# Kernel optimization log

Hardware: AMD Instinct MI355X
Metric: run time of the kernel (lower is better)

## Reference

```python
import jax, jax.numpy as jnp
import numpy as np

DECAY = 0.99
EPS = 1e-12  # torch F.normalize eps


def setup_inputs() -> dict:
    key = jax.random.key(0)
    ks = jax.random.split(key, 5)
    B, S, H, M = 4, 4096, 1024, 256
    x = jax.random.normal(ks[0], (B, S, H), dtype=jnp.float32)
    Wq = jax.random.normal(ks[1], (M, H), dtype=jnp.float32) * (H ** -0.5)
    Wk = jax.random.normal(ks[2], (M, H), dtype=jnp.float32) * (H ** -0.5)
    Wv = jax.random.normal(ks[3], (M, H), dtype=jnp.float32) * (H ** -0.5)
    # original inits W_out to zeros; use small random weights so the baseline output is non-trivial
    Wo = jax.random.normal(ks[4], (H, M), dtype=jnp.float32) * (M ** -0.5)
    M0 = jnp.zeros((M, M), dtype=jnp.float32)
    return {"x": x, "Wq": Wq, "Wk": Wk, "Wv": Wv, "Wo": Wo, "M0": M0, "chunk_size": 64}


def _l2norm(t):
    return t / jnp.maximum(jnp.linalg.norm(t, axis=-1, keepdims=True), EPS)


def reference(x, Wq, Wk, Wv, Wo, M0, chunk_size):
    B, S, H = x.shape
    m = Wq.shape[0]
    q = jnp.einsum('bsh,mh->bsm', x, Wq)
    k = _l2norm(jnp.einsum('bsh,mh->bsm', x, Wk))
    v = _l2norm(jnp.einsum('bsh,mh->bsm', x, Wv))
    n_chunks = S // chunk_size
    # (n_chunks, B, c, m)
    qc = q.reshape(B, n_chunks, chunk_size, m).transpose(1, 0, 2, 3)
    kc = k.reshape(B, n_chunks, chunk_size, m).transpose(1, 0, 2, 3)
    vc = v.reshape(B, n_chunks, chunk_size, m).transpose(1, 0, 2, 3)
    decay_c = DECAY ** chunk_size
    scale = 1.0 / (B * chunk_size)

    def step(M, qkv):
        qch, kch, vch = qkv
        r = jnp.einsum('bcm,nm->bcn', qch, M)  # q @ M.T
        outer = jnp.einsum('bci,bcj->ij', vch, kch) * scale
        return decay_c * M + outer, r

    _, rs = jax.lax.scan(step, M0, (qc, kc, vc))  # rs: (n_chunks, B, c, m)
    retrieved = rs.transpose(1, 0, 2, 3).reshape(B, S, m)
    return jnp.einsum('bsm,hm->bsh', retrieved, Wo)
```

## Files before the change

### kernel.cpp

```cpp
#include <hip/hip_runtime.h>
#include <math.h>

#define BB 4
#define SS 4096
#define HH 1024
#define MM 256
#define CHUNK 64
#define NCHUNK 64
#define ROWS (BB*SS)
#define QKV_LD 768
#define DECAY_F 0.99

typedef unsigned short u16;
typedef __attribute__((ext_vector_type(8))) short bf16x8;
typedef __attribute__((ext_vector_type(8))) unsigned short u16x8;
typedef __attribute__((ext_vector_type(4))) float f32x4;

__device__ inline u16 f2b(float f) {
  union { float f; unsigned u; } v; v.f = f;
  unsigned r = v.u + 0x7FFF + ((v.u >> 16) & 1);
  return (u16)(r >> 16);
}
__device__ inline float b2f(u16 h) {
  union { unsigned u; float f; } v; v.u = ((unsigned)h) << 16; return v.f;
}

__device__ inline void gload16(const void* g, void* l) {
  __builtin_amdgcn_global_load_lds(
      (const __attribute__((address_space(1))) unsigned int*)g,
      (__attribute__((address_space(3))) unsigned int*)l, 16, 0, 0);
}

__global__ __launch_bounds__(256) void cast_x_kernel(const float* __restrict__ src,
                                                     u16* __restrict__ dst) {
  int i = blockIdx.x * 256 + threadIdx.x;
  float4 v = reinterpret_cast<const float4*>(src)[i];
  ushort4 o;
  o.x = f2b(v.x); o.y = f2b(v.y); o.z = f2b(v.z); o.w = f2b(v.w);
  reinterpret_cast<ushort4*>(dst)[i] = o;
}

__global__ __launch_bounds__(256) void cast_w_kernel(const float* __restrict__ Wq,
                                                     const float* __restrict__ Wk,
                                                     const float* __restrict__ Wv,
                                                     const float* __restrict__ Wo,
                                                     u16* __restrict__ Wqkv_b,
                                                     u16* __restrict__ Wo_b) {
  int b = blockIdx.x, which = b >> 8;
  int i = ((b & 255) << 8) + threadIdx.x;
  const float* src = which == 0 ? Wq : which == 1 ? Wk : which == 2 ? Wv : Wo;
  u16* dst = which < 3 ? Wqkv_b + which * (MM * HH) : Wo_b;
  float4 v = reinterpret_cast<const float4*>(src)[i];
  ushort4 o;
  o.x = f2b(v.x); o.y = f2b(v.y); o.z = f2b(v.z); o.w = f2b(v.w);
  reinterpret_cast<ushort4*>(dst)[i] = o;
}

#define M_STD_BF16 0
#define M_STD_F32  1
#define M_OUTER    2
#define M_RETR     3

template<int MODE>
__global__ __launch_bounds__(256) void gemm128(const u16* __restrict__ A,
                                               const u16* __restrict__ Bg,
                                               const float* __restrict__ Bf,
                                               void* __restrict__ Cv,
                                               int K, int lda, int ldb, int ldc,
                                               float scale) {
  __shared__ bf16x8 As[2][512];
  __shared__ bf16x8 Bs[2][512];
  const int tid = threadIdx.x, lane = tid & 63, wv = tid >> 6;
  const int wr = wv >> 1, wc = wv & 1;
  const int t = (MODE == M_OUTER || MODE == M_RETR) ? blockIdx.z : 0;

  int bx, by;
  if (MODE == M_STD_BF16 || MODE == M_STD_F32) {
    int gx = gridDim.x;
    int nwg = gx * gridDim.y;
    int lin = blockIdx.y * gx + blockIdx.x;
    int chunk = nwg >> 3;
    int orig = (lin & 7) * chunk + (lin >> 3);
    bx = orig % gx; by = orig / gx;
  } else { bx = blockIdx.x; by = blockIdx.y; }

  const int row0 = by * 128;
  const int col0 = bx * 128;
  const int NK = K >> 5;
  const float* Mt = (MODE == M_RETR) ? (Bf + (size_t)t * (MM * MM)) : nullptr;

  auto stage = [&](int ks, int buf) {
    int koff;
    if (MODE == M_OUTER) koff = ((ks >> 1) << 12) + t * CHUNK + ((ks & 1) << 5);
    else                 koff = ks << 5;
#pragma unroll
    for (int j = 0; j < 2; ++j) {
      int m = j * 4 + wv;
      int rf = m * 16 + (lane & 15);
      size_t arow;
      if (MODE == M_RETR)
        arow = (size_t)(2 * by + (rf >> 6)) * SS + (size_t)t * CHUNK + (rf & 63);
      else
        arow = (size_t)(row0 + rf);
      const u16* ga = A + arow * (size_t)lda + koff + ((lane >> 4) << 3);
      gload16(ga, &As[buf][m * 64]);
      if (MODE != M_RETR) {
        const u16* gb = Bg + (size_t)(col0 + rf) * ldb + koff + ((lane >> 4) << 3);
        gload16(gb, &Bs[buf][m * 64]);
      }
    }
    if (MODE == M_RETR) {
#pragma unroll
      for (int j = 0; j < 2; ++j) {
        int s = tid + j * 256;
        int n = (s >> 6) * 16 + (lane & 15);
        const float* gm = Mt + (size_t)(col0 + n) * MM + (ks << 5) + ((lane >> 4) << 3);
        float4 f0 = *reinterpret_cast<const float4*>(gm);
        float4 f1 = *reinterpret_cast<const float4*>(gm + 4);
        u16x8 h;
        h[0] = f2b(f0.x); h[1] = f2b(f0.y); h[2] = f2b(f0.z); h[3] = f2b(f0.w);
        h[4] = f2b(f1.x); h[5] = f2b(f1.y); h[6] = f2b(f1.z); h[7] = f2b(f1.w);
        *reinterpret_cast<u16x8*>(&Bs[buf][s]) = h;
      }
    }
  };

  f32x4 acc[4][4] = {};
  stage(0, 0);
  for (int ks = 0; ks < NK; ++ks) {
    __syncthreads();
    if (ks + 1 < NK) stage(ks + 1, (ks + 1) & 1);
    const int buf = ks & 1;
    bf16x8 af[4], bfr[4];
#pragma unroll
    for (int m = 0; m < 4; ++m) af[m] = As[buf][(wr * 4 + m) * 64 + lane];
#pragma unroll
    for (int n = 0; n < 4; ++n) bfr[n] = Bs[buf][(wc * 4 + n) * 64 + lane];
#pragma unroll
    for (int m = 0; m < 4; ++m)
#pragma unroll
      for (int n = 0; n < 4; ++n)
        acc[m][n] = __builtin_amdgcn_mfma_f32_16x16x32_bf16(af[m], bfr[n], acc[m][n], 0, 0, 0);
  }

  const int r4 = (lane >> 4) << 2;
  const int cc = lane & 15;
#pragma unroll
  for (int m = 0; m < 4; ++m)
#pragma unroll
    for (int n = 0; n < 4; ++n)
#pragma unroll
      for (int r = 0; r < 4; ++r) {
        int lr = wr * 64 + m * 16 + r4 + r;
        int lc = wc * 64 + n * 16 + cc;
        float vv = acc[m][n][r];
        if (MODE == M_STD_BF16) {
          ((u16*)Cv)[(size_t)(row0 + lr) * ldc + col0 + lc] = f2b(vv);
        } else if (MODE == M_STD_F32) {
          ((float*)Cv)[(size_t)(row0 + lr) * ldc + col0 + lc] = vv;
        } else if (MODE == M_OUTER) {
          ((float*)Cv)[(size_t)t * (MM * MM) + (size_t)(row0 + lr) * MM + col0 + lc] = vv * scale;
        } else {
          size_t rowg = (size_t)(2 * by + (lr >> 6)) * SS + (size_t)t * CHUNK + (lr & 63);
          ((u16*)Cv)[rowg * MM + col0 + lc] = f2b(vv);
        }
      }
}

__global__ __launch_bounds__(256) void l2normT_kernel(const u16* __restrict__ qkv,
                                                      u16* __restrict__ kT,
                                                      u16* __restrict__ vT) {
  __shared__ u16 T[256][72];
  __shared__ float ps[64][4];
  __shared__ float inv[64];
  const int tid = threadIdx.x;
  const int q = tid >> 6, rl = tid & 63;
  const int row0 = blockIdx.x * 64;
#pragma unroll 1
  for (int seg = 0; seg < 2; ++seg) {
    u16* dstT = seg ? vT : kT;
    const int segbase = 256 + seg * 256;
    float ss = 0.f;
#pragma unroll
    for (int i = 0; i < 8; ++i) {
      u16x8 v = *reinterpret_cast<const u16x8*>(
          qkv + (size_t)(row0 + rl) * QKV_LD + segbase + q * 64 + i * 8);
#pragma unroll
      for (int e = 0; e < 8; ++e) {
        float f = b2f(v[e]);
        ss += f * f;
        T[q * 64 + i * 8 + e][rl] = v[e];
      }
    }
    ps[rl][q] = ss;
    __syncthreads();
    if (tid < 64) {
      float s = ps[tid][0] + ps[tid][1] + ps[tid][2] + ps[tid][3];
      inv[tid] = 1.0f / fmaxf(sqrtf(s), 1e-12f);
    }
    __syncthreads();
#pragma unroll
    for (int p = 0; p < 8; ++p) {
      int c = p * 32 + q * 8 + (rl >> 3);
      int r0 = (rl & 7) * 8;
      u16x8 val = *reinterpret_cast<const u16x8*>(&T[c][r0]);
      u16x8 o;
#pragma unroll
      for (int e = 0; e < 8; ++e) o[e] = f2b(b2f(val[e]) * inv[r0 + e]);
      *reinterpret_cast<u16x8*>(dstT + (size_t)c * ROWS + row0 + r0) = o;
    }
    __syncthreads();
  }
}

__global__ __launch_bounds__(256) void prefix_kernel(float* __restrict__ outer,
                                                     const float* __restrict__ M0,
                                                     float decay_c) {
  int ij = blockIdx.x * 256 + threadIdx.x;
  float run = M0[ij];
  float pre[8];
#pragma unroll
  for (int d = 0; d < 8; ++d) pre[d] = outer[(size_t)d * (MM * MM) + ij];
#pragma unroll 1
  for (int tb = 0; tb < NCHUNK; tb += 8) {
#pragma unroll
    for (int d = 0; d < 8; ++d) {
      int tc = tb + d;
      float o = pre[d];
      if (tb + 8 < NCHUNK) pre[d] = outer[(size_t)(tc + 8) * (MM * MM) + ij];
      outer[(size_t)tc * (MM * MM) + ij] = run;
      run = decay_c * run + o;
    }
  }
}

extern "C" void kernel_launch(void* const* d_in, const int* in_sizes, int n_in,
                              void* d_out, int out_size, void* d_ws, size_t ws_size,
                              hipStream_t stream) {
  const float* x  = (const float*)d_in[0];
  const float* Wq = (const float*)d_in[1];
  const float* Wk = (const float*)d_in[2];
  const float* Wv = (const float*)d_in[3];
  const float* Wo = (const float*)d_in[4];
  const float* M0 = (const float*)d_in[5];
  float* out = (float*)d_out;

  char* ws = (char*)d_ws;
  u16*   xb     = (u16*)(ws);
  u16*   qkv_b  = (u16*)(ws + 33554432);
  u16*   Wqkv_b = (u16*)(ws + 58720256);
  u16*   Wo_b   = (u16*)(ws + 60293120);
  u16*   kT     = (u16*)(ws);
  u16*   vT     = (u16*)(ws + 8388608);
  float* outer  = (float*)(ws + 16777216);
  u16*   r_b    = (u16*)(ws);

  const float scale   = 1.0f / (BB * CHUNK);
  const float decay_c = (float)pow(DECAY_F, (double)CHUNK);
  dim3 blk(256);

  cast_x_kernel<<<(ROWS * HH / 4) / 256, blk, 0, stream>>>(x, xb);
  cast_w_kernel<<<1024, blk, 0, stream>>>(Wq, Wk, Wv, Wo, Wqkv_b, Wo_b);
  gemm128<M_STD_BF16><<<dim3(QKV_LD / 128, ROWS / 128), blk, 0, stream>>>(
      xb, Wqkv_b, nullptr, qkv_b, HH, HH, HH, QKV_LD, 0.f);
  l2normT_kernel<<<ROWS / 64, blk, 0, stream>>>(qkv_b, kT, vT);
  gemm128<M_OUTER><<<dim3(2, 2, NCHUNK), blk, 0, stream>>>(
      vT, kT, nullptr, outer, MM, ROWS, ROWS, MM, scale);
  prefix_kernel<<<(MM * MM) / 256, blk, 0, stream>>>(outer, M0, decay_c);
  gemm128<M_RETR><<<dim3(2, 2, NCHUNK), blk, 0, stream>>>(
      qkv_b, nullptr, outer, r_b, MM, QKV_LD, 0, MM, 0.f);
  gemm128<M_STD_F32><<<dim3(HH / 128, ROWS / 128), blk, 0, stream>>>(
      r_b, Wo_b, nullptr, out, MM, MM, MM, HH, 0.f);
}
```

Baseline: 157.1 us.

## Triple-buffer GEMM LDS staging and emit bf16 prefix states for retrieval

Each GEMM's shared-memory staging goes from double to triple buffering. The loop waits on vmcnt before a raw s_barrier, so loads for step ks+2 can overlap compute on step ks. The prefix kernel now writes the running memory states directly as bf16 into a separate buffer. The retrieval GEMM can then use the same async global-to-LDS bf16 load path for B, replacing the fp32 load plus in-kernel conversion. This raises LDS use per block, which may lower occupancy. It also depends on the vmcnt(4) count matching the number of outstanding loads per stage.

Measured after the change: 153.2 us. -2.5%, faster.

```diff
diff --git a/kernel.cpp b/kernel.cpp
--- a/kernel.cpp
+++ b/kernel.cpp
@@ -64,12 +64,11 @@
 template<int MODE>
 __global__ __launch_bounds__(256) void gemm128(const u16* __restrict__ A,
                                                const u16* __restrict__ Bg,
-                                               const float* __restrict__ Bf,
                                                void* __restrict__ Cv,
                                                int K, int lda, int ldb, int ldc,
                                                float scale) {
-  __shared__ bf16x8 As[2][512];
-  __shared__ bf16x8 Bs[2][512];
+  __shared__ bf16x8 As[3][512];
+  __shared__ bf16x8 Bs[3][512];
   const int tid = threadIdx.x, lane = tid & 63, wv = tid >> 6;
   const int wr = wv >> 1, wc = wv & 1;
   const int t = (MODE == M_OUTER || MODE == M_RETR) ? blockIdx.z : 0;
@@ -87,7 +86,7 @@
   const int row0 = by * 128;
   const int col0 = bx * 128;
   const int NK = K >> 5;
-  const float* Mt = (MODE == M_RETR) ? (Bf + (size_t)t * (MM * MM)) : nullptr;
+  const u16* Bbase = (MODE == M_RETR) ? (Bg + (size_t)t * (MM * MM)) : Bg;
 
   auto stage = [&](int ks, int buf) {
     int koff;
@@ -104,43 +103,32 @@
         arow = (size_t)(row0 + rf);
       const u16* ga = A + arow * (size_t)lda + koff + ((lane >> 4) << 3);
       gload16(ga, &As[buf][m * 64]);
-      if (MODE != M_RETR) {
-        const u16* gb = Bg + (size_t)(col0 + rf) * ldb + koff + ((lane >> 4) << 3);
-        gload16(gb, &Bs[buf][m * 64]);
-      }
-    }
-    if (MODE == M_RETR) {
-#pragma unroll
-      for (int j = 0; j < 2; ++j) {
-        int s = tid + j * 256;
-        int n = (s >> 6) * 16 + (lane & 15);
-        const float* gm = Mt + (size_t)(col0 + n) * MM + (ks << 5) + ((lane >> 4) << 3);
-        float4 f0 = *reinterpret_cast<const float4*>(gm);
-        float4 f1 = *reinterpret_cast<const float4*>(gm + 4);
-        u16x8 h;
-        h[0] = f2b(f0.x); h[1] = f2b(f0.y); h[2] = f2b(f0.z); h[3] = f2b(f0.w);
-        h[4] = f2b(f1.x); h[5] = f2b(f1.y); h[6] = f2b(f1.z); h[7] = f2b(f1.w);
-        *reinterpret_cast<u16x8*>(&Bs[buf][s]) = h;
-      }
+      const u16* gb = Bbase + (size_t)(col0 + rf) * ldb + koff + ((lane >> 4) << 3);
+      gload16(gb, &Bs[buf][m * 64]);
     }
   };
 
   f32x4 acc[4][4] = {};
   stage(0, 0);
+  stage(1, 1);
+  int rb = 0, sb = 2;
   for (int ks = 0; ks < NK; ++ks) {
-    __syncthreads();
-    if (ks + 1 < NK) stage(ks + 1, (ks + 1) & 1);
-    const int buf = ks & 1;
+    if (ks + 1 < NK) asm volatile("s_waitcnt vmcnt(4)" ::: "memory");
+    else             asm volatile("s_waitcnt vmcnt(0)" ::: "memory");
+    __builtin_amdgcn_s_barrier();
+    if (ks + 2 < NK) stage(ks + 2, sb);
     bf16x8 af[4], bfr[4];
 #pragma unroll
-    for (int m = 0; m < 4; ++m) af[m] = As[buf][(wr * 4 + m) * 64 + lane];
-#pragma unroll
-    for (int n = 0; n < 4; ++n) bfr[n] = Bs[buf][(wc * 4 + n) * 64 + lane];
+    for (int m = 0; m < 4; ++m) af[m] = As[rb][(wr * 4 + m) * 64 + lane];
+#pragma unroll
+    for (int n = 0; n < 4; ++n) bfr[n] = Bs[rb][(wc * 4 + n) * 64 + lane];
 #pragma unroll
     for (int m = 0; m < 4; ++m)
 #pragma unroll
       for (int n = 0; n < 4; ++n)
         acc[m][n] = __builtin_amdgcn_mfma_f32_16x16x32_bf16(af[m], bfr[n], acc[m][n], 0, 0, 0);
+    rb = (rb == 2) ? 0 : rb + 1;
+    sb = (sb == 2) ? 0 : sb + 1;
   }
 
   const int r4 = (lane >> 4) << 2;
@@ -213,8 +201,9 @@
   }
 }
 
-__global__ __launch_bounds__(256) void prefix_kernel(float* __restrict__ outer,
+__global__ __launch_bounds__(256) void prefix_kernel(const float* __restrict__ outer,
                                                      const float* __restrict__ M0,
+                                                     u16* __restrict__ Mprev_b,
                                                      float decay_c) {
   int ij = blockIdx.x * 256 + threadIdx.x;
   float run = M0[ij];
@@ -228,7 +217,7 @@
       int tc = tb + d;
       float o = pre[d];
       if (tb + 8 < NCHUNK) pre[d] = outer[(size_t)(tc + 8) * (MM * MM) + ij];
-      outer[(size_t)tc * (MM * MM) + ij] = run;
+      Mprev_b[(size_t)tc * (MM * MM) + ij] = f2b(run);
       run = decay_c * run + o;
     }
   }
@@ -246,14 +235,15 @@
   float* out = (float*)d_out;
 
   char* ws = (char*)d_ws;
-  u16*   xb     = (u16*)(ws);
-  u16*   qkv_b  = (u16*)(ws + 33554432);
-  u16*   Wqkv_b = (u16*)(ws + 58720256);
-  u16*   Wo_b   = (u16*)(ws + 60293120);
-  u16*   kT     = (u16*)(ws);
-  u16*   vT     = (u16*)(ws + 8388608);
-  float* outer  = (float*)(ws + 16777216);
-  u16*   r_b    = (u16*)(ws);
+  u16*   xb      = (u16*)(ws);
+  u16*   qkv_b   = (u16*)(ws + 33554432);
+  u16*   Wqkv_b  = (u16*)(ws + 58720256);
+  u16*   Wo_b    = (u16*)(ws + 60293120);
+  u16*   kT      = (u16*)(ws);
+  u16*   vT      = (u16*)(ws + 8388608);
+  float* outer   = (float*)(ws + 16777216);
+  u16*   Mprev_b = (u16*)(ws + 8388608);
+  u16*   r_b     = (u16*)(ws);
 
   const float scale   = 1.0f / (BB * CHUNK);
   const float decay_c = (float)pow(DECAY_F, (double)CHUNK);
@@ -262,13 +252,13 @@
   cast_x_kernel<<<(ROWS * HH / 4) / 256, blk, 0, stream>>>(x, xb);
   cast_w_kernel<<<1024, blk, 0, stream>>>(Wq, Wk, Wv, Wo, Wqkv_b, Wo_b);
   gemm128<M_STD_BF16><<<dim3(QKV_LD / 128, ROWS / 128), blk, 0, stream>>>(
-      xb, Wqkv_b, nullptr, qkv_b, HH, HH, HH, QKV_LD, 0.f);
+      xb, Wqkv_b, qkv_b, HH, HH, HH, QKV_LD, 0.f);
   l2normT_kernel<<<ROWS / 64, blk, 0, stream>>>(qkv_b, kT, vT);
   gemm128<M_OUTER><<<dim3(2, 2, NCHUNK), blk, 0, stream>>>(
-      vT, kT, nullptr, outer, MM, ROWS, ROWS, MM, scale);
-  prefix_kernel<<<(MM * MM) / 256, blk, 0, stream>>>(outer, M0, decay_c);
+      vT, kT, outer, MM, ROWS, ROWS, MM, scale);
+  prefix_kernel<<<(MM * MM) / 256, blk, 0, stream>>>(outer, M0, Mprev_b, decay_c);
   gemm128<M_RETR><<<dim3(2, 2, NCHUNK), blk, 0, stream>>>(
-      qkv_b, nullptr, outer, r_b, MM, QKV_LD, 0, MM, 0.f);
+      qkv_b, Mprev_b, r_b, MM, QKV_LD, MM, MM, 0.f);
   gemm128<M_STD_F32><<<dim3(HH / 128, ROWS / 128), blk, 0, stream>>>(
-      r_b, Wo_b, nullptr, out, MM, MM, MM, HH, 0.f);
-}
+      r_b, Wo_b, out, MM, MM, MM, HH, 0.f);
+}
```
